# Kernel optimization log

Measured on AMD Instinct MI355X. Metric: run time of the kernel, lower is better.

## Reference

```python
import jax, jax.numpy as jnp
import numpy as np
import math

N_RES, N_EDGE = 10000, 320000
C_S, C_Z, C_H, H, PQ, PV = 384, 128, 16, 12, 4, 8
INF, EPS = 1e5, 1e-8


def _lin(key, din, dout):
    k1, k2 = jax.random.split(key)
    w = jax.random.normal(k1, (din, dout), jnp.float32) * (1.0 / np.sqrt(din))
    b = jax.random.normal(k2, (dout,), jnp.float32) * 0.02
    return w, b


def setup_inputs() -> dict:
    key = jax.random.key(0)
    ks = jax.random.split(key, 16)
    s = jax.random.normal(ks[0], (N_RES, C_S), jnp.float32)
    z = jax.random.normal(ks[1], (N_EDGE, C_Z), jnp.float32)
    edge_index = jax.random.randint(ks[2], (2, N_EDGE), 0, N_RES, jnp.int32)
    rot = jnp.linalg.qr(jax.random.normal(ks[3], (N_RES, 3, 3), jnp.float32))[0]
    trans = jax.random.normal(ks[4], (N_RES, 3), jnp.float32)
    mask = jnp.ones((N_RES,), jnp.float32)
    wq, bq = _lin(ks[5], C_S, H * C_H)
    wkv, bkv = _lin(ks[6], C_S, 2 * H * C_H)
    wqp, bqp = _lin(ks[7], C_S, H * PQ * 3)
    wkvp, bkvp = _lin(ks[8], C_S, H * (PQ + PV) * 3)
    wb, bb = _lin(ks[9], C_Z, H)
    wdz, bdz = _lin(ks[10], C_Z, C_Z // 4)
    head_w = jax.random.normal(ks[11], (H,), jnp.float32) * 0.1
    wout, bout = _lin(ks[12], H * (C_Z // 4 + C_H + PV * 4), C_S)
    return dict(s=s, z=z, rot=rot, trans=trans, mask=mask, edge_index=edge_index,
                wq=wq, bq=bq, wkv=wkv, bkv=bkv, wqp=wqp, bqp=bqp, wkvp=wkvp, bkvp=bkvp,
                wb=wb, bb=bb, wdz=wdz, bdz=bdz, head_w=head_w, wout=wout, bout=bout)


def reference(s, z, rot, trans, mask, edge_index, wq, bq, wkv, bkv, wqp, bqp,
              wkvp, bkvp, wb, bb, wdz, bdz, head_w, wout, bout):
    n = s.shape[0]
    src, dst = edge_index[0], edge_index[1]  # key-side, query-side

    q = (s @ wq + bq).reshape(n, H, C_H)
    kv = (s @ wkv + bkv).reshape(n, H, 2 * C_H)
    k, v = kv[..., :C_H], kv[..., C_H:]

    def make_pts(x, p):
        # torch: split [n, H*p*3] into 3 chunks of H*p, stack on last dim -> [n, H*p, 3]
        x = jnp.stack(jnp.split(x, 3, axis=-1), axis=-1)
        x = jnp.einsum('nij,npj->npi', rot, x) + trans[:, None, :]  # global frame
        return x.reshape(n, H, p, 3)

    q_pts = make_pts(s @ wqp + bqp, PQ)                 # [n, H, PQ, 3]
    kv_pts = make_pts(s @ wkvp + bkvp, PQ + PV)
    k_pts, v_pts = kv_pts[..., :PQ, :], kv_pts[..., PQ:, :]

    b = z @ wb + bb                                      # [E, H]
    a = jnp.einsum('ehc,ehc->eh', q[dst], k[src]) * math.sqrt(1.0 / (3 * C_H))
    a = a + math.sqrt(1.0 / 3) * b

    disp = q_pts[dst] - k_pts[src]                       # [E, H, PQ, 3]
    hw = jax.nn.softplus(head_w) * math.sqrt(1.0 / (3 * (PQ * 9.0 / 2)))
    pt_att = -0.5 * jnp.einsum('ehp,h->eh', jnp.sum(disp * disp, axis=-1), hw)

    edge_mask = INF * (mask[src] * mask[dst] - 1.0)
    a = a + pt_att + edge_mask[:, None]

    # segment softmax over edges grouped by destination node
    m = jax.lax.stop_gradient(jax.ops.segment_max(a, dst, num_segments=n))
    ea = jnp.exp(a - m[dst])
    a = ea / (jax.ops.segment_sum(ea, dst, num_segments=n)[dst] + 1e-16)

    o = jax.ops.segment_sum(a[..., None] * v[src], dst, num_segments=n).reshape(n, -1)

    o_pt = jax.ops.segment_sum(a[..., None, None] * v_pts[src], dst, num_segments=n)  # [n,H,PV,3]
    o_pt = jnp.einsum('nji,nhpj->nhpi', rot, o_pt - trans[:, None, None, :])  # invert_apply
    o_pt_norm = jnp.sqrt(jnp.sum(o_pt * o_pt, axis=-1) + EPS).reshape(n, -1)
    o_pt = o_pt.reshape(n, H * PV, 3)

    pair_z = z @ wdz + bdz                               # [E, c_z//4]
    o_pair = jax.ops.segment_sum(a[..., None] * pair_z[:, None, :], dst,
                                 num_segments=n).reshape(n, -1)

    feats = jnp.concatenate([o, o_pt[..., 0], o_pt[..., 1], o_pt[..., 2],
                             o_pt_norm, o_pair], axis=-1)
    return feats @ wout + bout
```

## Files before the change

kernel.cpp:

```cpp
#include <hip/hip_runtime.h>
#include <hip/hip_bf16.h>
#include <math.h>

#define N_RESC 10000
#define N_EDGEC 320000
#define C_SC 384
#define C_ZC 128
#define AGG_D 864
#define FEAT_D 960
#define OUT_D 384

#define S1C 0.14433756729740643f
#define S2C 0.5773502691896258f
#define SHWC 0.13608276348795434f

__global__ void k_zero(int* cursor) {
    int i = blockIdx.x * 256 + threadIdx.x;
    if (i < N_RESC) cursor[i] = 0;
}

__global__ void k_hist(const int* __restrict__ ei, int* cursor) {
    int e = blockIdx.x * 256 + threadIdx.x;
    if (e < N_EDGEC) atomicAdd(&cursor[ei[N_EDGEC + e]], 1);
}

__global__ __launch_bounds__(1024) void k_scan(int* cursor, int* rowptr) {
    __shared__ int buf[1024];
    __shared__ int carry_s;
    int t = threadIdx.x;
    if (t == 0) carry_s = 0;
    __syncthreads();
    for (int ch = 0; ch < 10; ++ch) {
        int idx = ch * 1024 + t;
        int v = (idx < N_RESC) ? cursor[idx] : 0;
        buf[t] = v;
        __syncthreads();
        for (int off = 1; off < 1024; off <<= 1) {
            int x = (t >= off) ? buf[t - off] : 0;
            __syncthreads();
            buf[t] += x;
            __syncthreads();
        }
        int incl = buf[t];
        int excl = incl - v;
        int base = carry_s;
        int total = buf[1023];
        if (idx < N_RESC) { rowptr[idx] = base + excl; cursor[idx] = base + excl; }
        __syncthreads();
        if (t == 0) carry_s = base + total;
        __syncthreads();
    }
    if (t == 0) rowptr[N_RESC] = carry_s;
}

__global__ void k_scatter(const int* __restrict__ ei, int* cursor, int* csr,
                          int* src_csr, int* epos) {
    int e = blockIdx.x * 256 + threadIdx.x;
    if (e < N_EDGEC) {
        int d = ei[N_EDGEC + e];
        int s = ei[e];
        int pos = atomicAdd(&cursor[d], 1);
        csr[pos] = e;
        src_csr[pos] = s;
        epos[e] = pos;
    }
}

__global__ __launch_bounds__(256) void k_wpack(
    const float* __restrict__ wq, const float* __restrict__ bq,
    const float* __restrict__ wkv, const float* __restrict__ bkv,
    const float* __restrict__ wqp, const float* __restrict__ bqp,
    const float* __restrict__ wkvp, const float* __restrict__ bkvp,
    const float* __restrict__ wb, const float* __restrict__ bb,
    const float* __restrict__ wdz, const float* __restrict__ bdz,
    float* __restrict__ wpack, float* __restrict__ bpack,
    float* __restrict__ wzpack, float* __restrict__ bzpack) {
    int idx = blockIdx.x * 256 + threadIdx.x;
    if (idx < 384 * 1152) {
        int j = idx / 1152, c = idx % 1152;
        float v;
        if (c < 192)      v = wq[j * 192 + c];
        else if (c < 576) v = wkv[j * 384 + (c - 192)];
        else if (c < 720) v = wqp[j * 144 + (c - 576)];
        else              v = wkvp[j * 432 + (c - 720)];
        wpack[idx] = v;
    }
    if (idx < 1152) {
        float b;
        if (idx < 192)      b = bq[idx];
        else if (idx < 576) b = bkv[idx - 192];
        else if (idx < 720) b = bqp[idx - 576];
        else                b = bkvp[idx - 720];
        bpack[idx] = b;
    }
    if (idx < 128 * 48) {
        int j = idx / 48, c = idx % 48;
        float v = 0.f;
        if (c < 12)      v = wb[j * 12 + c];
        else if (c < 44) v = wdz[j * 32 + (c - 12)];
        wzpack[idx] = v;
    }
    if (idx < 48) {
        float b = 0.f;
        if (idx < 12)      b = bb[idx];
        else if (idx < 44) b = bdz[idx - 12];
        bzpack[idx] = b;
    }
}

#define BM 64
#define BN 128
#define BK 32
__global__ __launch_bounds__(256) void k_proj(const float* __restrict__ s,
    const float* __restrict__ wpack, const float* __restrict__ bpack,
    float* __restrict__ qh, float* __restrict__ kh, float* __restrict__ vh,
    float* __restrict__ praw) {
    __shared__ float sT[BK][BM + 4];
    __shared__ float wt[BK][BN];
    int t = threadIdx.x;
    int bm0 = blockIdx.x * BM;
    int bn0 = blockIdx.y * BN;
    int tcol = t & 31;
    int trow = t >> 5;
    int c0 = tcol * 4;
    int r0 = trow * 8;

    int srow = t >> 2;
    int skoff = (t & 3) * 8;
    int gsrow = min(bm0 + srow, N_RESC - 1);
    const float* srcp = s + (long)gsrow * C_SC + skoff;

    float acc[8][4];
    #pragma unroll
    for (int i = 0; i < 8; i++)
        #pragma unroll
        for (int j = 0; j < 4; j++) acc[i][j] = 0.f;

    for (int k0 = 0; k0 < C_SC; k0 += BK) {
        float4 sa = *(const float4*)(srcp + k0);
        float4 sb = *(const float4*)(srcp + k0 + 4);
        sT[skoff + 0][srow] = sa.x; sT[skoff + 1][srow] = sa.y;
        sT[skoff + 2][srow] = sa.z; sT[skoff + 3][srow] = sa.w;
        sT[skoff + 4][srow] = sb.x; sT[skoff + 5][srow] = sb.y;
        sT[skoff + 6][srow] = sb.z; sT[skoff + 7][srow] = sb.w;
        #pragma unroll
        for (int q = 0; q < 4; q++) {
            int kk = (t >> 5) + q * 8;
            *(float4*)&wt[kk][c0] =
                *(const float4*)(wpack + (long)(k0 + kk) * 1152 + bn0 + c0);
        }
        __syncthreads();
        #pragma unroll
        for (int k = 0; k < BK; k++) {
            float4 a0 = *(const float4*)&sT[k][r0];
            float4 a1 = *(const float4*)&sT[k][r0 + 4];
            float4 b  = *(const float4*)&wt[k][c0];
            float av0 = a0.x, av1 = a0.y, av2 = a0.z, av3 = a0.w;
            float av4 = a1.x, av5 = a1.y, av6 = a1.z, av7 = a1.w;
            acc[0][0] = fmaf(av0, b.x, acc[0][0]); acc[0][1] = fmaf(av0, b.y, acc[0][1]);
            acc[0][2] = fmaf(av0, b.z, acc[0][2]); acc[0][3] = fmaf(av0, b.w, acc[0][3]);
            acc[1][0] = fmaf(av1, b.x, acc[1][0]); acc[1][1] = fmaf(av1, b.y, acc[1][1]);
            acc[1][2] = fmaf(av1, b.z, acc[1][2]); acc[1][3] = fmaf(av1, b.w, acc[1][3]);
            acc[2][0] = fmaf(av2, b.x, acc[2][0]); acc[2][1] = fmaf(av2, b.y, acc[2][1]);
            acc[2][2] = fmaf(av2, b.z, acc[2][2]); acc[2][3] = fmaf(av2, b.w, acc[2][3]);
            acc[3][0] = fmaf(av3, b.x, acc[3][0]); acc[3][1] = fmaf(av3, b.y, acc[3][1]);
            acc[3][2] = fmaf(av3, b.z, acc[3][2]); acc[3][3] = fmaf(av3, b.w, acc[3][3]);
            acc[4][0] = fmaf(av4, b.x, acc[4][0]); acc[4][1] = fmaf(av4, b.y, acc[4][1]);
            acc[4][2] = fmaf(av4, b.z, acc[4][2]); acc[4][3] = fmaf(av4, b.w, acc[4][3]);
            acc[5][0] = fmaf(av5, b.x, acc[5][0]); acc[5][1] = fmaf(av5, b.y, acc[5][1]);
            acc[5][2] = fmaf(av5, b.z, acc[5][2]); acc[5][3] = fmaf(av5, b.w, acc[5][3]);
            acc[6][0] = fmaf(av6, b.x, acc[6][0]); acc[6][1] = fmaf(av6, b.y, acc[6][1]);
            acc[6][2] = fmaf(av6, b.z, acc[6][2]); acc[6][3] = fmaf(av6, b.w, acc[6][3]);
            acc[7][0] = fmaf(av7, b.x, acc[7][0]); acc[7][1] = fmaf(av7, b.y, acc[7][1]);
            acc[7][2] = fmaf(av7, b.z, acc[7][2]); acc[7][3] = fmaf(av7, b.w, acc[7][3]);
        }
        __syncthreads();
    }
    #pragma unroll
    for (int j = 0; j < 4; j++) {
        int c = bn0 + c0 + j;
        float bv = bpack[c];
        #pragma unroll
        for (int i = 0; i < 8; i++) {
            int n = bm0 + r0 + i;
            if (n < N_RESC) {
                float val = acc[i][j] + bv;
                if (c < 192) qh[(long)n * 192 + c] = val;
                else if (c < 576) {
                    int cc = c - 192; int h = cc >> 5, r = cc & 31;
                    if (r < 16) kh[(long)n * 192 + h * 16 + r] = val;
                    else        vh[(long)n * 192 + h * 16 + (r - 16)] = val;
                } else praw[(long)n * 576 + (c - 576)] = val;
            }
        }
    }
}

__global__ __launch_bounds__(192) void k_rot(const float* __restrict__ praw,
    const float* __restrict__ rot, const float* __restrict__ trans,
    float* __restrict__ qpts, float* __restrict__ kpts, float* __restrict__ vpts) {
    int n = blockIdx.x;
    int t = threadIdx.x;
    __shared__ float R[9], T[3];
    if (t < 9) R[t] = rot[n * 9 + t];
    if (t < 3) T[t] = trans[n * 3 + t];
    __syncthreads();
    const float* pr = praw + (long)n * 576;
    if (t < 48) {
        float x0 = pr[t], x1 = pr[48 + t], x2 = pr[96 + t];
        #pragma unroll
        for (int i = 0; i < 3; i++)
            qpts[(long)n * 144 + t * 3 + i] = R[i*3+0]*x0 + R[i*3+1]*x1 + R[i*3+2]*x2 + T[i];
    } else {
        int p = t - 48;
        float x0 = pr[144 + p], x1 = pr[288 + p], x2 = pr[432 + p];
        int h = p / 12, pp = p % 12;
        #pragma unroll
        for (int i = 0; i < 3; i++) {
            float val = R[i*3+0]*x0 + R[i*3+1]*x1 + R[i*3+2]*x2 + T[i];
            if (pp < 4) kpts[(long)n * 144 + (h * 4 + pp) * 3 + i] = val;
            else        vpts[(long)n * 288 + (h * 8 + (pp - 4)) * 3 + i] = val;
        }
    }
}

#define ZBM 128
__global__ __launch_bounds__(256) void k_zproj(const float* __restrict__ z,
    const int* __restrict__ epos,
    const float* __restrict__ wzpack, const float* __restrict__ bzpack,
    float* __restrict__ b_e, float* __restrict__ pairz) {
    __shared__ float zT[32][ZBM + 4];
    __shared__ float wl[128][48];
    int t = threadIdx.x;
    long e0 = (long)blockIdx.x * ZBM;
    int er = t & 31;
    int cg = t >> 5;
    int cb = cg * 6;

    #pragma unroll
    for (int q = 0; q < 6; q++) {
        int f = t + q * 256;
        int row = f / 12, c4 = f % 12;
        *(float4*)&wl[row][c4 * 4] = *(const float4*)(wzpack + row * 48 + c4 * 4);
    }

    float acc[4][6];
    #pragma unroll
    for (int i = 0; i < 4; i++)
        #pragma unroll
        for (int j = 0; j < 6; j++) acc[i][j] = 0.f;

    int r = t >> 1, ch2 = t & 1;
    const float* zp = z + (e0 + r) * C_ZC + ch2 * 16;

    for (int kc = 0; kc < 4; kc++) {
        __syncthreads();
        #pragma unroll
        for (int q = 0; q < 4; q++) {
            float4 v = *(const float4*)(zp + kc * 32 + q * 4);
            int kk = ch2 * 16 + q * 4;
            zT[kk + 0][r] = v.x; zT[kk + 1][r] = v.y;
            zT[kk + 2][r] = v.z; zT[kk + 3][r] = v.w;
        }
        __syncthreads();
        #pragma unroll
        for (int k = 0; k < 32; k++) {
            float4 zv = *(const float4*)&zT[k][er * 4];
            const float* wrow = &wl[kc * 32 + k][cb];
            float w0 = wrow[0], w1 = wrow[1], w2 = wrow[2];
            float w3 = wrow[3], w4 = wrow[4], w5 = wrow[5];
            acc[0][0] = fmaf(zv.x, w0, acc[0][0]); acc[0][1] = fmaf(zv.x, w1, acc[0][1]);
            acc[0][2] = fmaf(zv.x, w2, acc[0][2]); acc[0][3] = fmaf(zv.x, w3, acc[0][3]);
            acc[0][4] = fmaf(zv.x, w4, acc[0][4]); acc[0][5] = fmaf(zv.x, w5, acc[0][5]);
            acc[1][0] = fmaf(zv.y, w0, acc[1][0]); acc[1][1] = fmaf(zv.y, w1, acc[1][1]);
            acc[1][2] = fmaf(zv.y, w2, acc[1][2]); acc[1][3] = fmaf(zv.y, w3, acc[1][3]);
            acc[1][4] = fmaf(zv.y, w4, acc[1][4]); acc[1][5] = fmaf(zv.y, w5, acc[1][5]);
            acc[2][0] = fmaf(zv.z, w0, acc[2][0]); acc[2][1] = fmaf(zv.z, w1, acc[2][1]);
            acc[2][2] = fmaf(zv.z, w2, acc[2][2]); acc[2][3] = fmaf(zv.z, w3, acc[2][3]);
            acc[2][4] = fmaf(zv.z, w4, acc[2][4]); acc[2][5] = fmaf(zv.z, w5, acc[2][5]);
            acc[3][0] = fmaf(zv.w, w0, acc[3][0]); acc[3][1] = fmaf(zv.w, w1, acc[3][1]);
            acc[3][2] = fmaf(zv.w, w2, acc[3][2]); acc[3][3] = fmaf(zv.w, w3, acc[3][3]);
            acc[3][4] = fmaf(zv.w, w4, acc[3][4]); acc[3][5] = fmaf(zv.w, w5, acc[3][5]);
        }
    }

    float bz0 = bzpack[cb + 0], bz1 = bzpack[cb + 1], bz2 = bzpack[cb + 2];
    float bz3 = bzpack[cb + 3], bz4 = bzpack[cb + 4], bz5 = bzpack[cb + 5];
    #pragma unroll
    for (int ei = 0; ei < 4; ei++) {
        long pos = epos[e0 + er * 4 + ei];
        float o0 = acc[ei][0] + bz0, o1 = acc[ei][1] + bz1;
        float o2 = acc[ei][2] + bz2, o3 = acc[ei][3] + bz3;
        float o4 = acc[ei][4] + bz4, o5 = acc[ei][5] + bz5;
        if (cb < 12) {
            float* d = b_e + pos * 12 + cb;
            *(float2*)(d + 0) = make_float2(o0, o1);
            *(float2*)(d + 2) = make_float2(o2, o3);
            *(float2*)(d + 4) = make_float2(o4, o5);
        } else if (cb < 42) {
            float* d = pairz + pos * 32 + (cb - 12);
            *(float2*)(d + 0) = make_float2(o0, o1);
            *(float2*)(d + 2) = make_float2(o2, o3);
            *(float2*)(d + 4) = make_float2(o4, o5);
        } else {
            *(float2*)(pairz + pos * 32 + 30) = make_float2(o0, o1);
        }
    }
}

#define CAPL 256
__global__ __launch_bounds__(256) void k_logit(const int* __restrict__ rowptr,
    const int* __restrict__ src_csr,
    const float* __restrict__ qh, const float* __restrict__ kh,
    const float* __restrict__ qpts, const float* __restrict__ kpts,
    const float* __restrict__ mask, const float* __restrict__ head_w,
    const float* __restrict__ b_e, float* __restrict__ alog) {
    int n = blockIdx.x;
    int t = threadIdx.x;
    __shared__ float qf[192], qp[144], hws[12];
    __shared__ int slist[CAPL];
    if (t < 192) qf[t] = qh[(long)n * 192 + t];
    if (t < 144) qp[t] = qpts[(long)n * 144 + t];
    if (t < 12)  hws[t] = log1pf(expf(head_w[t])) * SHWC;
    float mdst = mask[n];
    int row0 = rowptr[n];
    int deg = rowptr[n + 1] - row0;
    int w = t >> 6, l = t & 63, c = l & 15, hq = l >> 4;
    for (int cs = 0; cs < deg; cs += CAPL) {
        int cnt = min(CAPL, deg - cs);
        __syncthreads();
        for (int i = t; i < cnt; i += 256) slist[i] = src_csr[row0 + cs + i];
        __syncthreads();
        for (int i = w * 2; i < cnt; i += 8) {
            int i1 = min(i + 1, cnt - 1);
            int s0 = slist[i], s1 = slist[i1];
            int pos0 = row0 + cs + i, pos1 = row0 + cs + i1;
            float em0 = 100000.0f * (mask[s0] * mdst - 1.0f);
            float em1 = 100000.0f * (mask[s1] * mdst - 1.0f);
            float kv0[3], kv1[3];
            #pragma unroll
            for (int tp = 0; tp < 3; tp++) {
                kv0[tp] = kh[(long)s0 * 192 + tp * 64 + l];
                kv1[tp] = kh[(long)s1 * 192 + tp * 64 + l];
            }
            float kp0[3] = {0.f,0.f,0.f}, kp1[3] = {0.f,0.f,0.f};
            if (c < 12) {
                #pragma unroll
                for (int tp = 0; tp < 3; tp++) {
                    int h = tp * 4 + hq;
                    kp0[tp] = kpts[(long)s0 * 144 + h * 12 + c];
                    kp1[tp] = kpts[(long)s1 * 144 + h * 12 + c];
                }
            }
            float be0[3] = {0.f,0.f,0.f}, be1[3] = {0.f,0.f,0.f};
            if (c == 0) {
                #pragma unroll
                for (int tp = 0; tp < 3; tp++) {
                    int h = tp * 4 + hq;
                    be0[tp] = b_e[(long)pos0 * 12 + h];
                    be1[tp] = b_e[(long)pos1 * 12 + h];
                }
            }
            #pragma unroll
            for (int tp = 0; tp < 3; tp++) {
                int h = tp * 4 + hq;
                float qfv = S1C * qf[h * 16 + c];
                float val0 = qfv * kv0[tp];
                float val1 = qfv * kv1[tp];
                if (c < 12) {
                    float qpv = qp[h * 12 + c];
                    float hw = -0.5f * hws[h];
                    float d0 = qpv - kp0[tp];
                    float d1 = qpv - kp1[tp];
                    val0 = fmaf(hw * d0, d0, val0);
                    val1 = fmaf(hw * d1, d1, val1);
                }
                val0 += __shfl_xor(val0, 8, 16); val1 += __shfl_xor(val1, 8, 16);
                val0 += __shfl_xor(val0, 4, 16); val1 += __shfl_xor(val1, 4, 16);
                val0 += __shfl_xor(val0, 2, 16); val1 += __shfl_xor(val1, 2, 16);
                val0 += __shfl_xor(val0, 1, 16); val1 += __shfl_xor(val1, 1, 16);
                if (c == 0) {
                    alog[(long)pos0 * 12 + h] = val0 + S2C * be0[tp] + em0;
                    if (i1 != i)
                        alog[(long)pos1 * 12 + h] = val1 + S2C * be1[tp] + em1;
                }
            }
        }
    }
}

#define CAPE 256
__global__ __launch_bounds__(256) void k_agg(const int* __restrict__ rowptr,
    const int* __restrict__ src_csr,
    const float* __restrict__ alog, const float* __restrict__ vh,
    const float* __restrict__ vpts, const float* __restrict__ pairz,
    float* __restrict__ agg) {
    int n = blockIdx.x;
    int t = threadIdx.x;
    __shared__ float red[16 * 12];
    __shared__ float mh[12], linv[12];
    __shared__ float al[CAPE * 12];
    __shared__ int sl_[CAPE];
    int row0 = rowptr[n];
    int deg = rowptr[n + 1] - row0;
    int g = t >> 4, l16 = t & 15;
    if (l16 < 12) {
        float lm = -1e30f;
        for (int i = g; i < deg; i += 16)
            lm = fmaxf(lm, alog[(long)(row0 + i) * 12 + l16]);
        red[g * 12 + l16] = lm;
    }
    __syncthreads();
    if (t < 12) {
        float m = -1e30f;
        for (int gg = 0; gg < 16; gg++) m = fmaxf(m, red[gg * 12 + t]);
        mh[t] = m;
    }
    __syncthreads();
    if (l16 < 12) {
        float m = mh[l16];
        float ls = 0.f;
        for (int i = g; i < deg; i += 16)
            ls += expf(alog[(long)(row0 + i) * 12 + l16] - m);
        red[g * 12 + l16] = ls;
    }
    __syncthreads();
    if (t < 12) {
        float ssum = 0.f;
        for (int gg = 0; gg < 16; gg++) ssum += red[gg * 12 + t];
        linv[t] = 1.f / (ssum + 1e-16f);
    }

    const float* base = nullptr;
    int scale = 0, hk = 0, use_e = 0;
    int comp = t * 4;
    if (comp < 192)      { base = vh + comp; scale = 192; hk = comp >> 4; }
    else if (comp < 480) { int idx = comp - 192; base = vpts + idx; scale = 288; hk = idx / 24; }
    else if (comp < 864) { int idx = comp - 480; base = pairz + (idx & 31); scale = 32; hk = idx >> 5; use_e = 1; }
    float4 acc = make_float4(0.f, 0.f, 0.f, 0.f);

    for (int cs = 0; cs < deg; cs += CAPE) {
        int cnt = min(CAPE, deg - cs);
        int p0 = row0 + cs;
        __syncthreads();
        for (int i = t; i < cnt * 12; i += 256) {
            int h = i % 12;
            al[i] = expf(alog[(long)p0 * 12 + i] - mh[h]) * linv[h];
        }
        for (int i = t; i < cnt; i += 256) sl_[i] = src_csr[p0 + i];
        __syncthreads();
        if (t < 216) {
            int i = 0;
            for (; i + 4 <= cnt; i += 4) {
                int i0 = use_e ? (p0 + i)     : sl_[i];
                int i1 = use_e ? (p0 + i + 1) : sl_[i+1];
                int i2 = use_e ? (p0 + i + 2) : sl_[i+2];
                int i3 = use_e ? (p0 + i + 3) : sl_[i+3];
                float4 v0 = *(const float4*)(base + (long)i0 * scale);
                float4 v1 = *(const float4*)(base + (long)i1 * scale);
                float4 v2 = *(const float4*)(base + (long)i2 * scale);
                float4 v3 = *(const float4*)(base + (long)i3 * scale);
                float w0 = al[i * 12 + hk];
                float w1 = al[(i+1) * 12 + hk];
                float w2 = al[(i+2) * 12 + hk];
                float w3 = al[(i+3) * 12 + hk];
                acc.x = fmaf(w0, v0.x, acc.x); acc.y = fmaf(w0, v0.y, acc.y);
                acc.z = fmaf(w0, v0.z, acc.z); acc.w = fmaf(w0, v0.w, acc.w);
                acc.x = fmaf(w1, v1.x, acc.x); acc.y = fmaf(w1, v1.y, acc.y);
                acc.z = fmaf(w1, v1.z, acc.z); acc.w = fmaf(w1, v1.w, acc.w);
                acc.x = fmaf(w2, v2.x, acc.x); acc.y = fmaf(w2, v2.y, acc.y);
                acc.z = fmaf(w2, v2.z, acc.z); acc.w = fmaf(w2, v2.w, acc.w);
                acc.x = fmaf(w3, v3.x, acc.x); acc.y = fmaf(w3, v3.y, acc.y);
                acc.z = fmaf(w3, v3.z, acc.z); acc.w = fmaf(w3, v3.w, acc.w);
            }
            for (; i < cnt; i++) {
                int ii = use_e ? (p0 + i) : sl_[i];
                float4 v = *(const float4*)(base + (long)ii * scale);
                float w = al[i * 12 + hk];
                acc.x = fmaf(w, v.x, acc.x); acc.y = fmaf(w, v.y, acc.y);
                acc.z = fmaf(w, v.z, acc.z); acc.w = fmaf(w, v.w, acc.w);
            }
        }
    }
    if (t < 216) *(float4*)(agg + (long)n * AGG_D + comp) = acc;
}

#define NT_F 8
__global__ __launch_bounds__(192) void k_feat(const float* __restrict__ agg,
    const float* __restrict__ rot, const float* __restrict__ trans,
    float* __restrict__ feats) {
    int t = threadIdx.x;
    int node0 = blockIdx.x * NT_F;
    for (int idx = t; idx < NT_F * 192; idx += 192) {
        int nt = idx / 192, c = idx % 192;
        feats[(long)(node0 + nt) * FEAT_D + c] = agg[(long)(node0 + nt) * AGG_D + c];
    }
    for (int idx = t; idx < NT_F * 96; idx += 192) {
        int nt = idx / 96, p = idx % 96;
        int n = node0 + nt;
        const float* a = agg + (long)n * AGG_D;
        float gx = a[192 + p * 3 + 0] - trans[n * 3 + 0];
        float gy = a[192 + p * 3 + 1] - trans[n * 3 + 1];
        float gz = a[192 + p * 3 + 2] - trans[n * 3 + 2];
        const float* R = rot + (long)n * 9;
        float lx = R[0] * gx + R[3] * gy + R[6] * gz;
        float ly = R[1] * gx + R[4] * gy + R[7] * gz;
        float lz = R[2] * gx + R[5] * gy + R[8] * gz;
        float* f = feats + (long)n * FEAT_D;
        f[192 + p] = lx;
        f[288 + p] = ly;
        f[384 + p] = lz;
        f[480 + p] = sqrtf(lx * lx + ly * ly + lz * lz + 1e-8f);
    }
    for (int idx = t; idx < NT_F * 384; idx += 192) {
        int nt = idx / 384, q = idx % 384;
        feats[(long)(node0 + nt) * FEAT_D + 576 + q] =
            agg[(long)(node0 + nt) * AGG_D + 480 + q];
    }
}

__global__ __launch_bounds__(256) void k_out(const float* __restrict__ feats,
    const float* __restrict__ wout, const float* __restrict__ bout,
    float* __restrict__ out) {
    __shared__ float sT[BK][BM + 4];
    __shared__ float wt[BK][BN];
    int t = threadIdx.x;
    int bm0 = blockIdx.x * BM;
    int bn0 = blockIdx.y * BN;
    int tcol = t & 31;
    int trow = t >> 5;
    int c0 = tcol * 4;
    int r0 = trow * 8;

    int srow = t >> 2;
    int skoff = (t & 3) * 8;
    int gsrow = min(bm0 + srow, N_RESC - 1);
    const float* srcp = feats + (long)gsrow * FEAT_D + skoff;

    float acc[8][4];
    #pragma unroll
    for (int i = 0; i < 8; i++)
        #pragma unroll
        for (int j = 0; j < 4; j++) acc[i][j] = 0.f;

    for (int k0 = 0; k0 < FEAT_D; k0 += BK) {
        float4 sa = *(const float4*)(srcp + k0);
        float4 sb = *(const float4*)(srcp + k0 + 4);
        sT[skoff + 0][srow] = sa.x; sT[skoff + 1][srow] = sa.y;
        sT[skoff + 2][srow] = sa.z; sT[skoff + 3][srow] = sa.w;
        sT[skoff + 4][srow] = sb.x; sT[skoff + 5][srow] = sb.y;
        sT[skoff + 6][srow] = sb.z; sT[skoff + 7][srow] = sb.w;
        #pragma unroll
        for (int q = 0; q < 4; q++) {
            int kk = (t >> 5) + q * 8;
            *(float4*)&wt[kk][c0] =
                *(const float4*)(wout + (long)(k0 + kk) * OUT_D + bn0 + c0);
        }
        __syncthreads();
        #pragma unroll
        for (int k = 0; k < BK; k++) {
            float4 a0 = *(const float4*)&sT[k][r0];
            float4 a1 = *(const float4*)&sT[k][r0 + 4];
            float4 b  = *(const float4*)&wt[k][c0];
            float av0 = a0.x, av1 = a0.y, av2 = a0.z, av3 = a0.w;
            float av4 = a1.x, av5 = a1.y, av6 = a1.z, av7 = a1.w;
            acc[0][0] = fmaf(av0, b.x, acc[0][0]); acc[0][1] = fmaf(av0, b.y, acc[0][1]);
            acc[0][2] = fmaf(av0, b.z, acc[0][2]); acc[0][3] = fmaf(av0, b.w, acc[0][3]);
            acc[1][0] = fmaf(av1, b.x, acc[1][0]); acc[1][1] = fmaf(av1, b.y, acc[1][1]);
            acc[1][2] = fmaf(av1, b.z, acc[1][2]); acc[1][3] = fmaf(av1, b.w, acc[1][3]);
            acc[2][0] = fmaf(av2, b.x, acc[2][0]); acc[2][1] = fmaf(av2, b.y, acc[2][1]);
            acc[2][2] = fmaf(av2, b.z, acc[2][2]); acc[2][3] = fmaf(av2, b.w, acc[2][3]);
            acc[3][0] = fmaf(av3, b.x, acc[3][0]); acc[3][1] = fmaf(av3, b.y, acc[3][1]);
            acc[3][2] = fmaf(av3, b.z, acc[3][2]); acc[3][3] = fmaf(av3, b.w, acc[3][3]);
            acc[4][0] = fmaf(av4, b.x, acc[4][0]); acc[4][1] = fmaf(av4, b.y, acc[4][1]);
            acc[4][2] = fmaf(av4, b.z, acc[4][2]); acc[4][3] = fmaf(av4, b.w, acc[4][3]);
            acc[5][0] = fmaf(av5, b.x, acc[5][0]); acc[5][1] = fmaf(av5, b.y, acc[5][1]);
            acc[5][2] = fmaf(av5, b.z, acc[5][2]); acc[5][3] = fmaf(av5, b.w, acc[5][3]);
            acc[6][0] = fmaf(av6, b.x, acc[6][0]); acc[6][1] = fmaf(av6, b.y, acc[6][1]);
            acc[6][2] = fmaf(av6, b.z, acc[6][2]); acc[6][3] = fmaf(av6, b.w, acc[6][3]);
            acc[7][0] = fmaf(av7, b.x, acc[7][0]); acc[7][1] = fmaf(av7, b.y, acc[7][1]);
            acc[7][2] = fmaf(av7, b.z, acc[7][2]); acc[7][3] = fmaf(av7, b.w, acc[7][3]);
        }
        __syncthreads();
    }
    float bv0 = bout[bn0 + c0 + 0];
    float bv1 = bout[bn0 + c0 + 1];
    float bv2 = bout[bn0 + c0 + 2];
    float bv3 = bout[bn0 + c0 + 3];
    #pragma unroll
    for (int i = 0; i < 8; i++) {
        int n = bm0 + r0 + i;
        if (n < N_RESC) {
            *(float4*)(out + (long)n * OUT_D + bn0 + c0) =
                make_float4(acc[i][0] + bv0, acc[i][1] + bv1,
                            acc[i][2] + bv2, acc[i][3] + bv3);
        }
    }
}

extern "C" void kernel_launch(void* const* d_in, const int* in_sizes, int n_in,
                              void* d_out, int out_size, void* d_ws, size_t ws_size,
                              hipStream_t stream) {
    const float* s     = (const float*)d_in[0];
    const float* z     = (const float*)d_in[1];
    const float* rot   = (const float*)d_in[2];
    const float* trans = (const float*)d_in[3];
    const float* mask  = (const float*)d_in[4];
    const int*   ei    = (const int*)d_in[5];
    const float* wq    = (const float*)d_in[6];
    const float* bq    = (const float*)d_in[7];
    const float* wkv   = (const float*)d_in[8];
    const float* bkv   = (const float*)d_in[9];
    const float* wqp   = (const float*)d_in[10];
    const float* bqp   = (const float*)d_in[11];
    const float* wkvp  = (const float*)d_in[12];
    const float* bkvp  = (const float*)d_in[13];
    const float* wb    = (const float*)d_in[14];
    const float* bb    = (const float*)d_in[15];
    const float* wdz   = (const float*)d_in[16];
    const float* bdz   = (const float*)d_in[17];
    const float* head_w= (const float*)d_in[18];
    const float* wout  = (const float*)d_in[19];
    const float* bout  = (const float*)d_in[20];
    float* out = (float*)d_out;

    float* ws    = (float*)d_ws;
    float* qh    = ws;
    float* kh    = qh + 1920000;
    float* vh    = kh + 1920000;
    float* qpts  = vh + 1920000;
    float* kpts  = qpts + 1440000;
    float* vpts  = kpts + 1440000;
    float* b_e   = vpts + 2880000;
    float* pairz = b_e + 3840000;
    float* alog  = pairz + 10240000;
    float* agg   = alog + 3840000;
    float* praw  = agg;
    float* wpack = agg + 5760000;
    float* bpack = wpack + 442368;
    float* wzpack= bpack + 1152;
    float* bzpack= wzpack + 6144;
    float* feats = pairz;
    int* rowptr  = (int*)(agg + 8640000);
    int* cursor  = rowptr + 10004;
    int* csr     = cursor + 10000;
    int* src_csr = csr + N_EDGEC;
    int* epos    = src_csr + N_EDGEC;

    k_zero<<<(N_RESC + 255) / 256, 256, 0, stream>>>(cursor);
    k_hist<<<(N_EDGEC + 255) / 256, 256, 0, stream>>>(ei, cursor);
    k_scan<<<1, 1024, 0, stream>>>(cursor, rowptr);
    k_scatter<<<(N_EDGEC + 255) / 256, 256, 0, stream>>>(ei, cursor, csr, src_csr, epos);

    k_wpack<<<(384 * 1152 + 255) / 256, 256, 0, stream>>>(wq, bq, wkv, bkv, wqp, bqp,
                                                          wkvp, bkvp, wb, bb, wdz, bdz,
                                                          wpack, bpack, wzpack, bzpack);
    dim3 pgrid((N_RESC + BM - 1) / BM, 1152 / BN);
    k_proj<<<pgrid, 256, 0, stream>>>(s, wpack, bpack, qh, kh, vh, praw);
    k_rot<<<N_RESC, 192, 0, stream>>>(praw, rot, trans, qpts, kpts, vpts);

    k_zproj<<<N_EDGEC / ZBM, 256, 0, stream>>>(z, epos, wzpack, bzpack, b_e, pairz);

    k_logit<<<N_RESC, 256, 0, stream>>>(rowptr, src_csr, qh, kh, qpts, kpts,
                                        mask, head_w, b_e, alog);

    k_agg<<<N_RESC, 256, 0, stream>>>(rowptr, src_csr, alog, vh, vpts, pairz, agg);

    k_feat<<<N_RESC / NT_F, 192, 0, stream>>>(agg, rot, trans, feats);
    dim3 ogrid((N_RESC + BM - 1) / BM, OUT_D / BN);
    k_out<<<ogrid, 256, 0, stream>>>(feats, wout, bout, out);
}
```

Baseline: 768.5 us.

## Fuse logit and aggregation kernels with online softmax in shared memory

```diff
diff --git a/kernel.cpp b/kernel.cpp
--- a/kernel.cpp
+++ b/kernel.cpp
@@ -308,33 +308,49 @@
     }
 }
 
-#define CAPL 256
-__global__ __launch_bounds__(256) void k_logit(const int* __restrict__ rowptr,
+#define CAPA 256
+__global__ __launch_bounds__(256) void k_attn(const int* __restrict__ rowptr,
     const int* __restrict__ src_csr,
     const float* __restrict__ qh, const float* __restrict__ kh,
     const float* __restrict__ qpts, const float* __restrict__ kpts,
     const float* __restrict__ mask, const float* __restrict__ head_w,
-    const float* __restrict__ b_e, float* __restrict__ alog) {
+    const float* __restrict__ b_e,
+    const float* __restrict__ vh, const float* __restrict__ vpts,
+    const float* __restrict__ pairz,
+    float* __restrict__ agg) {
     int n = blockIdx.x;
     int t = threadIdx.x;
     __shared__ float qf[192], qp[144], hws[12];
-    __shared__ int slist[CAPL];
+    __shared__ int slist[CAPA];
+    __shared__ float al[CAPA * 12];
+    __shared__ float red[16 * 12];
+    __shared__ float mh[12], lh[12], rh[12];
     if (t < 192) qf[t] = qh[(long)n * 192 + t];
     if (t < 144) qp[t] = qpts[(long)n * 144 + t];
-    if (t < 12)  hws[t] = log1pf(expf(head_w[t])) * SHWC;
+    if (t < 12) { hws[t] = log1pf(expf(head_w[t])) * SHWC; mh[t] = -1e30f; lh[t] = 0.f; }
     float mdst = mask[n];
     int row0 = rowptr[n];
     int deg = rowptr[n + 1] - row0;
     int w = t >> 6, l = t & 63, c = l & 15, hq = l >> 4;
-    for (int cs = 0; cs < deg; cs += CAPL) {
-        int cnt = min(CAPL, deg - cs);
-        __syncthreads();
-        for (int i = t; i < cnt; i += 256) slist[i] = src_csr[row0 + cs + i];
+    int g = t >> 4, l16 = t & 15;
+
+    const float* base = nullptr;
+    int scale = 0, hk = 0, use_e = 0;
+    int comp = t * 4;
+    if (comp < 192)      { base = vh + comp; scale = 192; hk = comp >> 4; }
+    else if (comp < 480) { int idx = comp - 192; base = vpts + idx; scale = 288; hk = idx / 24; }
+    else if (comp < 864) { int idx = comp - 480; base = pairz + (idx & 31); scale = 32; hk = idx >> 5; use_e = 1; }
+    float4 acc = make_float4(0.f, 0.f, 0.f, 0.f);
+
+    for (int cs = 0; cs < deg; cs += CAPA) {
+        int cnt = min(CAPA, deg - cs);
+        int p0 = row0 + cs;
+        __syncthreads();
+        for (int i = t; i < cnt; i += 256) slist[i] = src_csr[p0 + i];
         __syncthreads();
         for (int i = w * 2; i < cnt; i += 8) {
             int i1 = min(i + 1, cnt - 1);
             int s0 = slist[i], s1 = slist[i1];
-            int pos0 = row0 + cs + i, pos1 = row0 + cs + i1;
             float em0 = 100000.0f * (mask[s0] * mdst - 1.0f);
             float em1 = 100000.0f * (mask[s1] * mdst - 1.0f);
             float kv0[3], kv1[3];
@@ -357,8 +373,8 @@
                 #pragma unroll
                 for (int tp = 0; tp < 3; tp++) {
                     int h = tp * 4 + hq;
-                    be0[tp] = b_e[(long)pos0 * 12 + h];
-                    be1[tp] = b_e[(long)pos1 * 12 + h];
+                    be0[tp] = b_e[(long)(p0 + i) * 12 + h];
+                    be1[tp] = b_e[(long)(p0 + i1) * 12 + h];
                 }
             }
             #pragma unroll
@@ -380,82 +396,52 @@
                 val0 += __shfl_xor(val0, 2, 16); val1 += __shfl_xor(val1, 2, 16);
                 val0 += __shfl_xor(val0, 1, 16); val1 += __shfl_xor(val1, 1, 16);
                 if (c == 0) {
-                    alog[(long)pos0 * 12 + h] = val0 + S2C * be0[tp] + em0;
+                    al[i * 12 + h] = val0 + S2C * be0[tp] + em0;
                     if (i1 != i)
-                        alog[(long)pos1 * 12 + h] = val1 + S2C * be1[tp] + em1;
+                        al[i1 * 12 + h] = val1 + S2C * be1[tp] + em1;
                 }
             }
         }
-    }
-}
-
-#define CAPE 256
-__global__ __launch_bounds__(256) void k_agg(const int* __restrict__ rowptr,
-    const int* __restrict__ src_csr,
-    const float* __restrict__ alog, const float* __restrict__ vh,
-    const float* __restrict__ vpts, const float* __restrict__ pairz,
-    float* __restrict__ agg) {
-    int n = blockIdx.x;
-    int t = threadIdx.x;
-    __shared__ float red[16 * 12];
-    __shared__ float mh[12], linv[12];
-    __shared__ float al[CAPE * 12];
-    __shared__ int sl_[CAPE];
-    int row0 = rowptr[n];
-    int deg = rowptr[n + 1] - row0;
-    int g = t >> 4, l16 = t & 15;
-    if (l16 < 12) {
-        float lm = -1e30f;
-        for (int i = g; i < deg; i += 16)
-            lm = fmaxf(lm, alog[(long)(row0 + i) * 12 + l16]);
-        red[g * 12 + l16] = lm;
-    }
-    __syncthreads();
-    if (t < 12) {
-        float m = -1e30f;
-        for (int gg = 0; gg < 16; gg++) m = fmaxf(m, red[gg * 12 + t]);
-        mh[t] = m;
-    }
-    __syncthreads();
-    if (l16 < 12) {
-        float m = mh[l16];
-        float ls = 0.f;
-        for (int i = g; i < deg; i += 16)
-            ls += expf(alog[(long)(row0 + i) * 12 + l16] - m);
-        red[g * 12 + l16] = ls;
-    }
-    __syncthreads();
-    if (t < 12) {
-        float ssum = 0.f;
-        for (int gg = 0; gg < 16; gg++) ssum += red[gg * 12 + t];
-        linv[t] = 1.f / (ssum + 1e-16f);
-    }
-
-    const float* base = nullptr;
-    int scale = 0, hk = 0, use_e = 0;
-    int comp = t * 4;
-    if (comp < 192)      { base = vh + comp; scale = 192; hk = comp >> 4; }
-    else if (comp < 480) { int idx = comp - 192; base = vpts + idx; scale = 288; hk = idx / 24; }
-    else if (comp < 864) { int idx = comp - 480; base = pairz + (idx & 31); scale = 32; hk = idx >> 5; use_e = 1; }
-    float4 acc = make_float4(0.f, 0.f, 0.f, 0.f);
-
-    for (int cs = 0; cs < deg; cs += CAPE) {
-        int cnt = min(CAPE, deg - cs);
-        int p0 = row0 + cs;
-        __syncthreads();
-        for (int i = t; i < cnt * 12; i += 256) {
-            int h = i % 12;
-            al[i] = expf(alog[(long)p0 * 12 + i] - mh[h]) * linv[h];
-        }
-        for (int i = t; i < cnt; i += 256) sl_[i] = src_csr[p0 + i];
+        __syncthreads();
+        if (l16 < 12) {
+            float lm = -1e30f;
+            for (int i = g; i < cnt; i += 16) lm = fmaxf(lm, al[i * 12 + l16]);
+            red[g * 12 + l16] = lm;
+        }
+        __syncthreads();
+        if (t < 12) {
+            float m = mh[t];
+            for (int gg = 0; gg < 16; gg++) m = fmaxf(m, red[gg * 12 + t]);
+            rh[t] = expf(mh[t] - m);
+            mh[t] = m;
+        }
+        __syncthreads();
+        if (l16 < 12) {
+            float m = mh[l16];
+            float ls = 0.f;
+            for (int i = g; i < cnt; i += 16) {
+                float p = expf(al[i * 12 + l16] - m);
+                al[i * 12 + l16] = p;
+                ls += p;
+            }
+            red[g * 12 + l16] = ls;
+        }
+        __syncthreads();
+        if (t < 12) {
+            float ss = 0.f;
+            for (int gg = 0; gg < 16; gg++) ss += red[gg * 12 + t];
+            lh[t] = lh[t] * rh[t] + ss;
+        }
         __syncthreads();
         if (t < 216) {
+            float r = rh[hk];
+            acc.x *= r; acc.y *= r; acc.z *= r; acc.w *= r;
             int i = 0;
             for (; i + 4 <= cnt; i += 4) {
-                int i0 = use_e ? (p0 + i)     : sl_[i];
-                int i1 = use_e ? (p0 + i + 1) : sl_[i+1];
-                int i2 = use_e ? (p0 + i + 2) : sl_[i+2];
-                int i3 = use_e ? (p0 + i + 3) : sl_[i+3];
+                int i0 = use_e ? (p0 + i)     : slist[i];
+                int i1 = use_e ? (p0 + i + 1) : slist[i+1];
+                int i2 = use_e ? (p0 + i + 2) : slist[i+2];
+                int i3 = use_e ? (p0 + i + 3) : slist[i+3];
                 float4 v0 = *(const float4*)(base + (long)i0 * scale);
                 float4 v1 = *(const float4*)(base + (long)i1 * scale);
                 float4 v2 = *(const float4*)(base + (long)i2 * scale);
@@ -474,15 +460,19 @@
                 acc.z = fmaf(w3, v3.z, acc.z); acc.w = fmaf(w3, v3.w, acc.w);
             }
             for (; i < cnt; i++) {
-                int ii = use_e ? (p0 + i) : sl_[i];
+                int ii = use_e ? (p0 + i) : slist[i];
                 float4 v = *(const float4*)(base + (long)ii * scale);
-                float w = al[i * 12 + hk];
-                acc.x = fmaf(w, v.x, acc.x); acc.y = fmaf(w, v.y, acc.y);
-                acc.z = fmaf(w, v.z, acc.z); acc.w = fmaf(w, v.w, acc.w);
-            }
-        }
-    }
-    if (t < 216) *(float4*)(agg + (long)n * AGG_D + comp) = acc;
+                float wv = al[i * 12 + hk];
+                acc.x = fmaf(wv, v.x, acc.x); acc.y = fmaf(wv, v.y, acc.y);
+                acc.z = fmaf(wv, v.z, acc.z); acc.w = fmaf(wv, v.w, acc.w);
+            }
+        }
+    }
+    if (t < 216) {
+        float linv = 1.f / (lh[hk] + 1e-16f);
+        acc.x *= linv; acc.y *= linv; acc.z *= linv; acc.w *= linv;
+        *(float4*)(agg + (long)n * AGG_D + comp) = acc;
+    }
 }
 
 #define NT_F 8
@@ -661,10 +651,8 @@
 
     k_zproj<<<N_EDGEC / ZBM, 256, 0, stream>>>(z, epos, wzpack, bzpack, b_e, pairz);
 
-    k_logit<<<N_RESC, 256, 0, stream>>>(rowptr, src_csr, qh, kh, qpts, kpts,
-                                        mask, head_w, b_e, alog);
-
-    k_agg<<<N_RESC, 256, 0, stream>>>(rowptr, src_csr, alog, vh, vpts, pairz, agg);
+    k_attn<<<N_RESC, 256, 0, stream>>>(rowptr, src_csr, qh, kh, qpts, kpts,
+                                       mask, head_w, b_e, vh, vpts, pairz, agg);
 
     k_feat<<<N_RESC / NT_F, 192, 0, stream>>>(agg, rot, trans, feats);
     dim3 ogrid((N_RESC + BM - 1) / BM, OUT_D / BN);
```

Result: no change. 767.1 us (-0.2%).
